# Kernel optimization log

Measured on AMD Instinct MI355X. Metric: run time of the kernel, lower is better.

## Reference

```python
import jax, jax.numpy as jnp
import numpy as np

D_IN = 768
D_MODEL = 768
NUM_HEADS = 12
DEPTH = D_MODEL // NUM_HEADS


def setup_inputs() -> dict:
    key = jax.random.key(0)
    ks = jax.random.split(key, 9)
    B, N = 2, 2048
    s_in = 1.0 / np.sqrt(D_IN)
    s_md = 1.0 / np.sqrt(D_MODEL)
    return {
        "x": jax.random.normal(ks[0], (B, N, D_IN), dtype=jnp.float32),
        "wq": jax.random.normal(ks[1], (D_IN, D_MODEL), dtype=jnp.float32) * s_in,
        "bq": jax.random.normal(ks[2], (D_MODEL,), dtype=jnp.float32) * 0.02,
        "wk": jax.random.normal(ks[3], (D_IN, D_MODEL), dtype=jnp.float32) * s_in,
        "bk": jax.random.normal(ks[4], (D_MODEL,), dtype=jnp.float32) * 0.02,
        "wv": jax.random.normal(ks[5], (D_IN, D_MODEL), dtype=jnp.float32) * s_in,
        "bv": jax.random.normal(ks[6], (D_MODEL,), dtype=jnp.float32) * 0.02,
        "wo": jax.random.normal(ks[7], (D_MODEL, D_MODEL), dtype=jnp.float32) * s_md,
        "bo": jax.random.normal(ks[8], (D_MODEL,), dtype=jnp.float32) * 0.02,
    }


def reference(x, wq, bq, wk, bk, wv, bv, wo, bo):
    B, N, _ = x.shape
    H, D = NUM_HEADS, DEPTH
    # project and split heads: [B,N,H,D] -> [B,H,N,D]
    q = (x @ wq + bq).reshape(B, N, H, D).transpose(0, 2, 1, 3)
    k = (x @ wk + bk).reshape(B, N, H, D).transpose(0, 2, 1, 3)
    v = (x @ wv + bv).reshape(B, N, H, D).transpose(0, 2, 1, 3)
    scale = 1.0 / jnp.sqrt(jnp.asarray(D, dtype=q.dtype))
    attn = jnp.einsum('bhnd,bhmd->bhnm', q, k) * scale  # [B,H,N,N]
    attn = jax.nn.softmax(attn, axis=-1)
    z = jnp.einsum('bhnm,bhmd->bhnd', attn, v)
    z = z.transpose(0, 2, 1, 3).reshape(B, N, H * D)
    return z @ wo + bo
```

## Files before the change

### kernel.cpp

```cpp
#include <hip/hip_runtime.h>
#include <hip/hip_bf16.h>
#include <math.h>

#define NH 12
#define DH 64
#define BB 2
#define NN 2048
#define DM 768

typedef short v8s __attribute__((ext_vector_type(8)));
typedef float v4f __attribute__((ext_vector_type(4)));

__device__ __forceinline__ unsigned short f2bf(float f) {
    union { float f; unsigned u; } x; x.f = f;
    unsigned r = x.u + 0x7fffu + ((x.u >> 16) & 1u);
    return (unsigned short)(r >> 16);
}

__device__ __forceinline__ int cvtpk(float lo, float hi2) {
    int r;
    asm("v_cvt_pk_bf16_f32 %0, %1, %2" : "=v"(r) : "v"(lo), "v"(hi2));
    return r;
}

__device__ __forceinline__ void glds16(const void* g, void* l) {
    __builtin_amdgcn_global_load_lds((const __attribute__((address_space(1))) void*)g,
                                     (__attribute__((address_space(3))) void*)l, 16, 0, 0);
}

__global__ __launch_bounds__(256) void cast_x_k(const float* __restrict__ in,
                                                unsigned short* __restrict__ out, int n) {
    int i = (blockIdx.x * 256 + threadIdx.x) * 4;
    if (i >= n) return;
    float4 v = *(const float4*)(in + i);
    ushort4 o;
    o.x = f2bf(v.x); o.y = f2bf(v.y); o.z = f2bf(v.z); o.w = f2bf(v.w);
    *(ushort4*)(out + i) = o;
}

__global__ __launch_bounds__(256) void cast_wT_k(const float* __restrict__ w0, const float* __restrict__ w1,
                                                 const float* __restrict__ w2, const float* __restrict__ w3,
                                                 unsigned short* __restrict__ o0, unsigned short* __restrict__ o1,
                                                 unsigned short* __restrict__ o2, unsigned short* __restrict__ o3) {
    __shared__ unsigned short t[64][65];
    const float* in; unsigned short* out;
    switch (blockIdx.y) {
        case 0: in = w0; out = o0; break;
        case 1: in = w1; out = o1; break;
        case 2: in = w2; out = o2; break;
        default: in = w3; out = o3; break;
    }
    int kt = blockIdx.x / 12, ct = blockIdx.x % 12;
    int rr = threadIdx.x >> 4, cc = threadIdx.x & 15;
#pragma unroll
    for (int it = 0; it < 4; it++) {
        int row = kt * 64 + it * 16 + rr;
        int col = ct * 64 + cc * 4;
        float4 v = *(const float4*)(in + row * 768 + col);
        t[it * 16 + rr][cc * 4 + 0] = f2bf(v.x);
        t[it * 16 + rr][cc * 4 + 1] = f2bf(v.y);
        t[it * 16 + rr][cc * 4 + 2] = f2bf(v.z);
        t[it * 16 + rr][cc * 4 + 3] = f2bf(v.w);
    }
    __syncthreads();
#pragma unroll
    for (int it = 0; it < 4; it++) {
        int c_l = it * 16 + rr;
        int k_l = cc * 4;
        ushort4 o;
        o.x = t[k_l + 0][c_l];
        o.y = t[k_l + 1][c_l];
        o.z = t[k_l + 2][c_l];
        o.w = t[k_l + 3][c_l];
        *(ushort4*)(out + (ct * 64 + c_l) * 768 + kt * 64 + k_l) = o;
    }
}

__global__ __launch_bounds__(256) void qkv_gemm_k(
    const unsigned short* __restrict__ xb,
    const unsigned short* __restrict__ wqT, const unsigned short* __restrict__ wkT,
    const unsigned short* __restrict__ wvT,
    const float* __restrict__ bq, const float* __restrict__ bk, const float* __restrict__ bv,
    unsigned short* __restrict__ q, unsigned short* __restrict__ k, unsigned short* __restrict__ vT) {
    __shared__ unsigned short Abuf[3][128 * 32];
    __shared__ unsigned short Bbuf[3][128 * 32];

    int ctile = blockIdx.x;
    int mtile = blockIdx.y;
    int mat = ctile / 6;
    int col0 = (ctile % 6) * 128;
    const unsigned short* Bsrc = (mat == 0) ? wqT : ((mat == 1) ? wkT : wvT);
    const float* bias = (mat == 0) ? bq : ((mat == 1) ? bk : bv);

    int tid = threadIdx.x;
    int w = tid >> 6, l = tid & 63;
    int q16 = l & 15, g = l >> 4;
    int wr = w >> 1, wc = w & 1;

    int srow0 = tid >> 2;
    int ss = tid & 3;

    auto stage = [&](int tt, int buf) {
        int k0 = tt * 32;
#pragma unroll
        for (int i = 0; i < 2; ++i) {
            int row = srow0 + i * 64;
            int c16 = ss ^ ((row >> 1) & 3);
            glds16(xb + (mtile * 128 + row) * 768 + k0 + (c16 << 3),
                   (char*)&Abuf[buf][0] + i * 4096 + tid * 16);
            glds16(Bsrc + (col0 + row) * 768 + k0 + (c16 << 3),
                   (char*)&Bbuf[buf][0] + i * 4096 + tid * 16);
        }
    };

    v4f zero = {0.f, 0.f, 0.f, 0.f};
    v4f acc[4][4];
#pragma unroll
    for (int i = 0; i < 4; i++)
#pragma unroll
        for (int j = 0; j < 4; j++) acc[i][j] = zero;

    stage(0, 0);
    stage(1, 1);
    asm volatile("s_waitcnt vmcnt(4)" ::: "memory");
    __builtin_amdgcn_s_barrier();
    asm volatile("" ::: "memory");

    int rd = 0;
    for (int tt = 0; tt < 24; ++tt) {
        int st = rd + 2; if (st >= 3) st -= 3;
        if (tt + 2 < 24) stage(tt + 2, st);
        const char* Ab = (const char*)&Abuf[rd][0];
        const char* Bb = (const char*)&Bbuf[rd][0];
        v8s af[4], bf[4];
#pragma unroll
        for (int f = 0; f < 4; f++) {
            int arow = wr * 64 + f * 16 + q16;
            af[f] = *(const v8s*)(Ab + arow * 64 + ((g ^ ((arow >> 1) & 3)) << 4));
            int brow = wc * 64 + f * 16 + q16;
            bf[f] = *(const v8s*)(Bb + brow * 64 + ((g ^ ((brow >> 1) & 3)) << 4));
        }
#pragma unroll
        for (int i = 0; i < 4; i++)
#pragma unroll
            for (int j = 0; j < 4; j++)
                acc[i][j] = __builtin_amdgcn_mfma_f32_16x16x32_bf16(af[i], bf[j], acc[i][j], 0, 0, 0);
        asm volatile("s_waitcnt vmcnt(4)" ::: "memory");
        __builtin_amdgcn_s_barrier();
        asm volatile("" ::: "memory");
        rd = (rd + 1 == 3) ? 0 : rd + 1;
    }

    const float QSCL = 0.125f * 1.44269504088896340736f;
#pragma unroll
    for (int i = 0; i < 4; i++)
#pragma unroll
        for (int j = 0; j < 4; j++)
#pragma unroll
            for (int r = 0; r < 4; r++) {
                int gr = mtile * 128 + wr * 64 + i * 16 + 4 * g + r;
                int gcl = col0 + wc * 64 + j * 16 + q16;
                int b = gr / NN, n = gr % NN;
                int h = gcl / DH, d = gcl % DH;
                int bh = b * NH + h;
                float v = acc[i][j][r] + bias[gcl];
                if (mat == 0)      q[(bh * NN + n) * DH + d]  = f2bf(v * QSCL);
                else if (mat == 1) k[(bh * NN + n) * DH + d]  = f2bf(v);
                else               vT[(bh * DH + d) * NN + n] = f2bf(v);
            }
}

__global__ __launch_bounds__(256) void attn_k(
    const unsigned short* __restrict__ q, const unsigned short* __restrict__ k,
    const unsigned short* __restrict__ vT, unsigned short* __restrict__ z) {
    __shared__ unsigned short Kbuf[2][64 * 64];
    __shared__ unsigned short Vbuf[2][64 * 64];
    __shared__ unsigned short plds[4][16][72];

    int bh = blockIdx.x % 24;
    int qt = blockIdx.x / 24;
    int b = bh / NH, h = bh % NH;
    int w = threadIdx.x >> 6, l = threadIdx.x & 63;
    int q16 = l & 15, g = l >> 4;
    const unsigned short* qp = q + (size_t)bh * NN * DH;
    const unsigned short* kp = k + (size_t)bh * NN * DH;
    const unsigned short* vp = vT + (size_t)bh * DH * NN;
    int qrow = qt * 64 + w * 16 + q16;

    v8s qf0 = *(const v8s*)(qp + qrow * DH + 8 * g);
    v8s qf1 = *(const v8s*)(qp + qrow * DH + 32 + 8 * g);

    v8s ones;
#pragma unroll
    for (int i = 0; i < 8; i++) ones[i] = (short)0x3F80;

    int sY = w * 2048 + l * 16;
    int srow0 = sY >> 7;
    int ss = (sY >> 4) & 7;

    auto stage = [&](int t, int buf) {
        int kv = t * 64;
#pragma unroll
        for (int i = 0; i < 2; ++i) {
            int row = srow0 + i * 8;
            int c16 = ss ^ (row & 7);
            char* kdst = (char*)&Kbuf[buf][0] + w * 2048 + i * 1024;
            char* vdst = (char*)&Vbuf[buf][0] + w * 2048 + i * 1024;
            glds16(kp + (kv + row) * DH + (c16 << 3), kdst);
            glds16(vp + row * NN + kv + (c16 << 3), vdst);
        }
    };

    v4f zero = {0.f, 0.f, 0.f, 0.f};
    float mrow = -INFINITY;
    v4f o[4];
    v4f osum = zero;
#pragma unroll
    for (int dt = 0; dt < 4; dt++) o[dt] = zero;

    stage(0, 0);
    __syncthreads();

    for (int t = 0; t < NN / 64; ++t) {
        int cur = t & 1;
        if (t + 1 < NN / 64) stage(t + 1, cur ^ 1);

        const char* kb = (const char*)&Kbuf[cur][0];
        const char* vb = (const char*)&Vbuf[cur][0];

        v4f st[4];
#pragma unroll
        for (int ct = 0; ct < 4; ct++) {
            int krow = ct * 16 + q16;
            v8s kf0 = *(const v8s*)(kb + krow * 128 + ((g ^ (krow & 7)) << 4));
            v8s kf1 = *(const v8s*)(kb + krow * 128 + (((4 + g) ^ (krow & 7)) << 4));
            st[ct] = __builtin_amdgcn_mfma_f32_16x16x32_bf16(kf0, qf0, zero, 0, 0, 0);
            st[ct] = __builtin_amdgcn_mfma_f32_16x16x32_bf16(kf1, qf1, st[ct], 0, 0, 0);
        }

        float ma = fmaxf(fmaxf(st[0][0], st[0][1]), st[0][2]);
        float mb = fmaxf(fmaxf(st[0][3], st[1][0]), st[1][1]);
        float mc = fmaxf(fmaxf(st[1][2], st[1][3]), st[2][0]);
        float md = fmaxf(fmaxf(st[2][1], st[2][2]), st[2][3]);
        float me = fmaxf(fmaxf(st[3][0], st[3][1]), st[3][2]);
        float vmax = fmaxf(fmaxf(ma, mb), mc);
        vmax = fmaxf(fmaxf(vmax, md), fmaxf(me, st[3][3]));
        vmax = fmaxf(vmax, __shfl_xor(vmax, 16));
        vmax = fmaxf(vmax, __shfl_xor(vmax, 32));

        if (!__all(vmax <= mrow + 8.f)) {
            float mn = fmaxf(mrow, vmax);
            float sc = exp2f(mrow - mn);
#pragma unroll
            for (int dt = 0; dt < 4; dt++)
#pragma unroll
                for (int r = 0; r < 4; r++) o[dt][r] *= sc;
            osum[0] *= sc;
            mrow = mn;
        }

#pragma unroll
        for (int ct = 0; ct < 4; ct++) {
            float p0 = exp2f(st[ct][0] - mrow);
            float p1 = exp2f(st[ct][1] - mrow);
            float p2 = exp2f(st[ct][2] - mrow);
            float p3 = exp2f(st[ct][3] - mrow);
            union { int i[2]; short4 s; } u;
            u.i[0] = cvtpk(p0, p1);
            u.i[1] = cvtpk(p2, p3);
            *(short4*)(&plds[w][q16][ct * 16 + 4 * g]) = u.s;
        }

        v8s pf0 = *(const v8s*)(&plds[w][q16][8 * g]);
        v8s pf1 = *(const v8s*)(&plds[w][q16][32 + 8 * g]);

        osum = __builtin_amdgcn_mfma_f32_16x16x32_bf16(ones, pf0, osum, 0, 0, 0);
        osum = __builtin_amdgcn_mfma_f32_16x16x32_bf16(ones, pf1, osum, 0, 0, 0);

#pragma unroll
        for (int dt = 0; dt < 4; dt++) {
            int dcol = dt * 16 + q16;
            v8s vf0 = *(const v8s*)(vb + dcol * 128 + ((g ^ (dcol & 7)) << 4));
            v8s vf1 = *(const v8s*)(vb + dcol * 128 + (((4 + g) ^ (dcol & 7)) << 4));
            o[dt] = __builtin_amdgcn_mfma_f32_16x16x32_bf16(vf0, pf0, o[dt], 0, 0, 0);
            o[dt] = __builtin_amdgcn_mfma_f32_16x16x32_bf16(vf1, pf1, o[dt], 0, 0, 0);
        }
        __syncthreads();
    }

    float inv = 1.f / osum[0];
    int n = qt * 64 + w * 16 + q16;
#pragma unroll
    for (int dt = 0; dt < 4; dt++) {
        short4 s4;
        s4.x = (short)f2bf(o[dt][0] * inv);
        s4.y = (short)f2bf(o[dt][1] * inv);
        s4.z = (short)f2bf(o[dt][2] * inv);
        s4.w = (short)f2bf(o[dt][3] * inv);
        *(short4*)(&z[((size_t)(b * NN + n)) * DM + h * DH + dt * 16 + 4 * g]) = s4;
    }
}

__global__ __launch_bounds__(256) void out_gemm_k(
    const unsigned short* __restrict__ zb, const unsigned short* __restrict__ woT,
    const float* __restrict__ bo, float* __restrict__ out) {
    __shared__ unsigned short Abuf[3][128 * 32];
    __shared__ unsigned short Bbuf[3][128 * 32];

    int ctile = blockIdx.x;
    int mtile = blockIdx.y;
    int col0 = ctile * 128;

    int tid = threadIdx.x;
    int w = tid >> 6, l = tid & 63;
    int q16 = l & 15, g = l >> 4;
    int wr = w >> 1, wc = w & 1;

    int srow0 = tid >> 2;
    int ss = tid & 3;

    auto stage = [&](int tt, int buf) {
        int k0 = tt * 32;
#pragma unroll
        for (int i = 0; i < 2; ++i) {
            int row = srow0 + i * 64;
            int c16 = ss ^ ((row >> 1) & 3);
            glds16(zb + (mtile * 128 + row) * 768 + k0 + (c16 << 3),
                   (char*)&Abuf[buf][0] + i * 4096 + tid * 16);
            glds16(woT + (col0 + row) * 768 + k0 + (c16 << 3),
                   (char*)&Bbuf[buf][0] + i * 4096 + tid * 16);
        }
    };

    v4f zero = {0.f, 0.f, 0.f, 0.f};
    v4f acc[4][4];
#pragma unroll
    for (int i = 0; i < 4; i++)
#pragma unroll
        for (int j = 0; j < 4; j++) acc[i][j] = zero;

    stage(0, 0);
    stage(1, 1);
    asm volatile("s_waitcnt vmcnt(4)" ::: "memory");
    __builtin_amdgcn_s_barrier();
    asm volatile("" ::: "memory");

    int rd = 0;
    for (int tt = 0; tt < 24; ++tt) {
        int st = rd + 2; if (st >= 3) st -= 3;
        if (tt + 2 < 24) stage(tt + 2, st);
        const char* Ab = (const char*)&Abuf[rd][0];
        const char* Bb = (const char*)&Bbuf[rd][0];
        v8s af[4], bf[4];
#pragma unroll
        for (int f = 0; f < 4; f++) {
            int arow = wr * 64 + f * 16 + q16;
            af[f] = *(const v8s*)(Ab + arow * 64 + ((g ^ ((arow >> 1) & 3)) << 4));
            int brow = wc * 64 + f * 16 + q16;
            bf[f] = *(const v8s*)(Bb + brow * 64 + ((g ^ ((brow >> 1) & 3)) << 4));
        }
#pragma unroll
        for (int i = 0; i < 4; i++)
#pragma unroll
            for (int j = 0; j < 4; j++)
                acc[i][j] = __builtin_amdgcn_mfma_f32_16x16x32_bf16(af[i], bf[j], acc[i][j], 0, 0, 0);
        asm volatile("s_waitcnt vmcnt(4)" ::: "memory");
        __builtin_amdgcn_s_barrier();
        asm volatile("" ::: "memory");
        rd = (rd + 1 == 3) ? 0 : rd + 1;
    }

#pragma unroll
    for (int i = 0; i < 4; i++)
#pragma unroll
        for (int j = 0; j < 4; j++)
#pragma unroll
            for (int r = 0; r < 4; r++) {
                int gr = mtile * 128 + wr * 64 + i * 16 + 4 * g + r;
                int gc = col0 + wc * 64 + j * 16 + q16;
                out[gr * 768 + gc] = acc[i][j][r] + bo[gc];
            }
}

extern "C" void kernel_launch(void* const* d_in, const int* in_sizes, int n_in,
                              void* d_out, int out_size, void* d_ws, size_t ws_size,
                              hipStream_t stream) {
    const float* x  = (const float*)d_in[0];
    const float* wq = (const float*)d_in[1];
    const float* bq = (const float*)d_in[2];
    const float* wk = (const float*)d_in[3];
    const float* bk = (const float*)d_in[4];
    const float* wv = (const float*)d_in[5];
    const float* bv = (const float*)d_in[6];
    const float* wo = (const float*)d_in[7];
    const float* bo = (const float*)d_in[8];
    float* out = (float*)d_out;

    const int NX = BB * NN * DM;
    const int NW = 768 * 768;

    unsigned short* wsp = (unsigned short*)d_ws;
    unsigned short* xb  = wsp;
    unsigned short* wqT = xb + NX;
    unsigned short* wkT = wqT + NW;
    unsigned short* wvT = wkT + NW;
    unsigned short* woT = wvT + NW;
    unsigned short* qb  = woT + NW;
    unsigned short* kb  = qb + NX;
    unsigned short* vTb = kb + NX;
    unsigned short* zb  = vTb + NX;

    cast_x_k<<<NX / (256 * 4), 256, 0, stream>>>(x, xb, NX);
    cast_wT_k<<<dim3(144, 4), 256, 0, stream>>>(wq, wk, wv, wo, wqT, wkT, wvT, woT);
    qkv_gemm_k<<<dim3(18, 32), 256, 0, stream>>>(xb, wqT, wkT, wvT, bq, bk, bv, qb, kb, vTb);
    attn_k<<<BB * NH * (NN / 64), 256, 0, stream>>>(qb, kb, vTb, zb);
    out_gemm_k<<<dim3(6, 32), 256, 0, stream>>>(zb, woT, bo, out);
}
```

Baseline: 130.7 us.

## Split attention KV sequence across two wave groups with in-block softmax merge

The attention block grows from 256 to 512 threads. Two groups of four waves each process half of the key/value sequence, using 32-wide KV tiles, and the partial outputs, maxima and sums are merged through shared memory at the end. The aim is to double the waves per block and shorten each wave's serial loop, improving latency hiding and occupancy on the CU. In exchange it adds a final reduction with an extra barrier, uses smaller MFMA K per iteration with a relatively higher softmax overhead, and changes the shared-memory swizzle.

```diff
diff --git a/kernel.cpp b/kernel.cpp
--- a/kernel.cpp
+++ b/kernel.cpp
@@ -170,22 +170,25 @@
             }
 }
 
-__global__ __launch_bounds__(256) void attn_k(
+__global__ __launch_bounds__(512) void attn_k(
     const unsigned short* __restrict__ q, const unsigned short* __restrict__ k,
     const unsigned short* __restrict__ vT, unsigned short* __restrict__ z) {
-    __shared__ unsigned short Kbuf[2][64 * 64];
-    __shared__ unsigned short Vbuf[2][64 * 64];
-    __shared__ unsigned short plds[4][16][72];
+    __shared__ __align__(16) char Kb[2][2][4096];
+    __shared__ __align__(16) char Vb[2][2][4096];
+    __shared__ unsigned short plds[8][16][36];
 
     int bh = blockIdx.x % 24;
     int qt = blockIdx.x / 24;
     int b = bh / NH, h = bh % NH;
-    int w = threadIdx.x >> 6, l = threadIdx.x & 63;
+    int tid = threadIdx.x;
+    int w = tid >> 6, l = tid & 63;
     int q16 = l & 15, g = l >> 4;
+    int ws = w & 3, hf = w >> 2;
+
     const unsigned short* qp = q + (size_t)bh * NN * DH;
     const unsigned short* kp = k + (size_t)bh * NN * DH;
     const unsigned short* vp = vT + (size_t)bh * DH * NN;
-    int qrow = qt * 64 + w * 16 + q16;
+    int qrow = qt * 64 + ws * 16 + q16;
 
     v8s qf0 = *(const v8s*)(qp + qrow * DH + 8 * g);
     v8s qf1 = *(const v8s*)(qp + qrow * DH + 32 + 8 * g);
@@ -194,21 +197,17 @@
 #pragma unroll
     for (int i = 0; i < 8; i++) ones[i] = (short)0x3F80;
 
-    int sY = w * 2048 + l * 16;
-    int srow0 = sY >> 7;
-    int ss = (sY >> 4) & 7;
+    int hf_s = tid >> 8;
+    int s8 = tid & 255;
+    int krow_s = s8 >> 3, ksl = s8 & 7;
+    int kc16 = ksl ^ (krow_s & 7);
+    int vrow_s = s8 >> 2, vsl = s8 & 3;
+    int vc16 = vsl ^ (vrow_s & 3);
 
     auto stage = [&](int t, int buf) {
-        int kv = t * 64;
-#pragma unroll
-        for (int i = 0; i < 2; ++i) {
-            int row = srow0 + i * 8;
-            int c16 = ss ^ (row & 7);
-            char* kdst = (char*)&Kbuf[buf][0] + w * 2048 + i * 1024;
-            char* vdst = (char*)&Vbuf[buf][0] + w * 2048 + i * 1024;
-            glds16(kp + (kv + row) * DH + (c16 << 3), kdst);
-            glds16(vp + row * NN + kv + (c16 << 3), vdst);
-        }
+        int kv0 = hf_s * (NN / 2) + t * 32;
+        glds16(kp + (kv0 + krow_s) * DH + (kc16 << 3), &Kb[hf_s][buf][s8 * 16]);
+        glds16(vp + (size_t)vrow_s * NN + kv0 + (vc16 << 3), &Vb[hf_s][buf][s8 * 16]);
     };
 
     v4f zero = {0.f, 0.f, 0.f, 0.f};
@@ -221,16 +220,16 @@
     stage(0, 0);
     __syncthreads();
 
-    for (int t = 0; t < NN / 64; ++t) {
+    for (int t = 0; t < 32; ++t) {
         int cur = t & 1;
-        if (t + 1 < NN / 64) stage(t + 1, cur ^ 1);
-
-        const char* kb = (const char*)&Kbuf[cur][0];
-        const char* vb = (const char*)&Vbuf[cur][0];
-
-        v4f st[4];
-#pragma unroll
-        for (int ct = 0; ct < 4; ct++) {
+        if (t + 1 < 32) stage(t + 1, cur ^ 1);
+
+        const char* kb = &Kb[hf][cur][0];
+        const char* vb = &Vb[hf][cur][0];
+
+        v4f st[2];
+#pragma unroll
+        for (int ct = 0; ct < 2; ct++) {
             int krow = ct * 16 + q16;
             v8s kf0 = *(const v8s*)(kb + krow * 128 + ((g ^ (krow & 7)) << 4));
             v8s kf1 = *(const v8s*)(kb + krow * 128 + (((4 + g) ^ (krow & 7)) << 4));
@@ -240,11 +239,7 @@
 
         float ma = fmaxf(fmaxf(st[0][0], st[0][1]), st[0][2]);
         float mb = fmaxf(fmaxf(st[0][3], st[1][0]), st[1][1]);
-        float mc = fmaxf(fmaxf(st[1][2], st[1][3]), st[2][0]);
-        float md = fmaxf(fmaxf(st[2][1], st[2][2]), st[2][3]);
-        float me = fmaxf(fmaxf(st[3][0], st[3][1]), st[3][2]);
-        float vmax = fmaxf(fmaxf(ma, mb), mc);
-        vmax = fmaxf(fmaxf(vmax, md), fmaxf(me, st[3][3]));
+        float vmax = fmaxf(fmaxf(ma, mb), fmaxf(st[1][2], st[1][3]));
         vmax = fmaxf(vmax, __shfl_xor(vmax, 16));
         vmax = fmaxf(vmax, __shfl_xor(vmax, 32));
 
@@ -260,7 +255,7 @@
         }
 
 #pragma unroll
-        for (int ct = 0; ct < 4; ct++) {
+        for (int ct = 0; ct < 2; ct++) {
             float p0 = exp2f(st[ct][0] - mrow);
             float p1 = exp2f(st[ct][1] - mrow);
             float p2 = exp2f(st[ct][2] - mrow);
@@ -272,32 +267,47 @@
         }
 
         v8s pf0 = *(const v8s*)(&plds[w][q16][8 * g]);
-        v8s pf1 = *(const v8s*)(&plds[w][q16][32 + 8 * g]);
 
         osum = __builtin_amdgcn_mfma_f32_16x16x32_bf16(ones, pf0, osum, 0, 0, 0);
-        osum = __builtin_amdgcn_mfma_f32_16x16x32_bf16(ones, pf1, osum, 0, 0, 0);
 
 #pragma unroll
         for (int dt = 0; dt < 4; dt++) {
             int dcol = dt * 16 + q16;
-            v8s vf0 = *(const v8s*)(vb + dcol * 128 + ((g ^ (dcol & 7)) << 4));
-            v8s vf1 = *(const v8s*)(vb + dcol * 128 + (((4 + g) ^ (dcol & 7)) << 4));
-            o[dt] = __builtin_amdgcn_mfma_f32_16x16x32_bf16(vf0, pf0, o[dt], 0, 0, 0);
-            o[dt] = __builtin_amdgcn_mfma_f32_16x16x32_bf16(vf1, pf1, o[dt], 0, 0, 0);
+            v8s vf = *(const v8s*)(vb + dcol * 64 + ((g ^ (dcol & 3)) << 4));
+            o[dt] = __builtin_amdgcn_mfma_f32_16x16x32_bf16(vf, pf0, o[dt], 0, 0, 0);
         }
         __syncthreads();
     }
 
-    float inv = 1.f / osum[0];
-    int n = qt * 64 + w * 16 + q16;
-#pragma unroll
-    for (int dt = 0; dt < 4; dt++) {
-        short4 s4;
-        s4.x = (short)f2bf(o[dt][0] * inv);
-        s4.y = (short)f2bf(o[dt][1] * inv);
-        s4.z = (short)f2bf(o[dt][2] * inv);
-        s4.w = (short)f2bf(o[dt][3] * inv);
-        *(short4*)(&z[((size_t)(b * NN + n)) * DM + h * DH + dt * 16 + 4 * g]) = s4;
+    float* po = (float*)&Kb[0][0][0];
+    float* pm = (float*)&Vb[0][0][0];
+    float* pl = pm + 64;
+    int row = ws * 16 + q16;
+
+    if (hf == 1) {
+#pragma unroll
+        for (int dt = 0; dt < 4; dt++)
+#pragma unroll
+            for (int r = 0; r < 4; r++)
+                po[row * 64 + dt * 16 + 4 * g + r] = o[dt][r];
+        if (g == 0) { pm[row] = mrow; pl[row] = osum[0]; }
+    }
+    __syncthreads();
+    if (hf == 0) {
+        float m1 = pm[row], l1 = pl[row];
+        float ms = fmaxf(mrow, m1);
+        float a0 = exp2f(mrow - ms), a1 = exp2f(m1 - ms);
+        float inv = 1.f / (osum[0] * a0 + l1 * a1);
+        int n = qt * 64 + ws * 16 + q16;
+#pragma unroll
+        for (int dt = 0; dt < 4; dt++) {
+            short4 s4;
+            s4.x = (short)f2bf((o[dt][0] * a0 + po[row * 64 + dt * 16 + 4 * g + 0] * a1) * inv);
+            s4.y = (short)f2bf((o[dt][1] * a0 + po[row * 64 + dt * 16 + 4 * g + 1] * a1) * inv);
+            s4.z = (short)f2bf((o[dt][2] * a0 + po[row * 64 + dt * 16 + 4 * g + 2] * a1) * inv);
+            s4.w = (short)f2bf((o[dt][3] * a0 + po[row * 64 + dt * 16 + 4 * g + 3] * a1) * inv);
+            *(short4*)(&z[((size_t)(b * NN + n)) * DM + h * DH + dt * 16 + 4 * g]) = s4;
+        }
     }
 }
 
@@ -413,6 +423,6 @@
     cast_x_k<<<NX / (256 * 4), 256, 0, stream>>>(x, xb, NX);
     cast_wT_k<<<dim3(144, 4), 256, 0, stream>>>(wq, wk, wv, wo, wqT, wkT, wvT, woT);
     qkv_gemm_k<<<dim3(18, 32), 256, 0, stream>>>(xb, wqT, wkT, wvT, bq, bk, bv, qb, kb, vTb);
-    attn_k<<<BB * NH * (NN / 64), 256, 0, stream>>>(qb, kb, vTb, zb);
+    attn_k<<<BB * NH * (NN / 64), 512, 0, stream>>>(qb, kb, vTb, zb);
     out_gemm_k<<<dim3(6, 32), 256, 0, stream>>>(zb, woT, bo, out);
 }
```

Result: faster. 125.0 us (-4.4%).
